# Performance work log

Measured on AMD Instinct MI355X. Metric: run time of the kernel, lower is better.

Reference implementation:

```python
import jax, jax.numpy as jnp
import numpy as np

B, S, D = 2, 2048, 1024
H_Q, H_KV, DK, DV = 16, 8, 64, 64
R = H_Q // H_KV  # q heads per kv head (GQA)
THETA = 10000.0


def setup_inputs() -> dict:
    key = jax.random.key(0)
    ks = jax.random.split(key, 12)
    inv_freq = 1.0 / (THETA ** (jnp.arange(0, DK, 2, dtype=jnp.float32) / DK))  # [DK/2]
    angles = jnp.arange(S, dtype=jnp.float32)[:, None] * inv_freq[None, :]      # [S, DK/2]
    scale = 0.02
    return {
        "x": jax.random.normal(ks[0], (B, S, D), jnp.float32),
        "Wq": jax.random.normal(ks[1], (D, H_Q * DK), jnp.float32) * scale,
        "bq": jnp.zeros((H_Q * DK,), jnp.float32),
        "Wk": jax.random.normal(ks[2], (D, H_KV * DK), jnp.float32) * scale,
        "bk": jnp.zeros((H_KV * DK,), jnp.float32),
        "Wv": jax.random.normal(ks[3], (D, H_KV * DV), jnp.float32) * scale,
        "bv": jnp.zeros((H_KV * DV,), jnp.float32),
        "Wo": jax.random.normal(ks[4], (H_Q * DV, D), jnp.float32) * scale,
        "bo": jnp.zeros((D,), jnp.float32),
        "freqs_cos": jnp.cos(angles),
        "freqs_sin": jnp.sin(angles),
        "attention_mask": jax.random.bernoulli(ks[5], 0.9, (B, S)),  # True = real token
    }


def _rope(t, cos, sin):
    # t: [B, S, H, Dh]; cos/sin: [S, Dh/2]. Complex rotation on interleaved pairs.
    tp = t.reshape(*t.shape[:-1], -1, 2)
    x1, x2 = tp[..., 0], tp[..., 1]
    c = cos[None, :, None, :]
    s = sin[None, :, None, :]
    o1 = x1 * c - x2 * s
    o2 = x1 * s + x2 * c
    return jnp.stack([o1, o2], axis=-1).reshape(t.shape)


def reference(x, Wq, bq, Wk, bk, Wv, bv, Wo, bo, freqs_cos, freqs_sin, attention_mask):
    b, s, _ = x.shape
    q = (x @ Wq + bq).reshape(b, s, H_Q, DK)
    k = (x @ Wk + bk).reshape(b, s, H_KV, DK)
    v = (x @ Wv + bv).reshape(b, s, H_KV, DV)
    q = _rope(q, freqs_cos, freqs_sin)
    k = _rope(k, freqs_cos, freqs_sin)
    q = q.transpose(0, 2, 1, 3)                      # [B, Hq, S, DK]
    k = jnp.repeat(k.transpose(0, 2, 1, 3), R, axis=1)  # GQA expand -> [B, Hq, S, DK]
    v = jnp.repeat(v.transpose(0, 2, 1, 3), R, axis=1)  # [B, Hq, S, DV]
    causal = jnp.tril(jnp.ones((s, s), dtype=bool))
    # Module does logical_or(padding, causal) -- replicated faithfully.
    mask = jnp.logical_or(attention_mask[:, None, None, :], causal[None, None])
    scale = 1.0 / jnp.sqrt(jnp.float32(DK))
    scores = jnp.einsum('bhqd,bhkd->bhqk', q, k) * scale
    scores = jnp.where(mask, scores, -jnp.inf)
    attn = jax.nn.softmax(scores, axis=-1)
    out = jnp.einsum('bhqk,bhkd->bhqd', attn, v)
    out = out.transpose(0, 2, 1, 3).reshape(b, s, H_Q * DV)
    return out @ Wo + bo
```

## Files before the change

### kernel.cpp

```cpp
#include <hip/hip_runtime.h>
#include <hip/hip_bf16.h>
#include <math.h>

typedef __attribute__((ext_vector_type(8))) short bf16x8;
typedef __attribute__((ext_vector_type(4))) float f32x4;

#define OFF_XB  0ull
#define OFF_WT  (8ull<<20)
#define OFF_WO  (12ull<<20)
#define OFF_QB  (14ull<<20)
#define OFF_KB  (22ull<<20)
#define OFF_VT  (26ull<<20)
#define OFF_AO  (30ull<<20)
#define OFF_MB  (38ull<<20)

#define QSCALE 0.18033688056680276f

__device__ inline unsigned pack_bf162(float a, float b) {
    __hip_bfloat162 t = __float22bfloat162_rn(make_float2(a, b));
    return *(unsigned*)&t;
}

__device__ inline float exp2_fast(float x) {
    float r;
    asm("v_exp_f32 %0, %1" : "=v"(r) : "v"(x));
    return r;
}

__device__ inline void gload16(const void* g, void* l) {
    __builtin_amdgcn_global_load_lds(
        (const __attribute__((address_space(1))) void*)g,
        (__attribute__((address_space(3))) void*)l, 16, 0, 0);
}

__launch_bounds__(256)
__global__ void prep_kernel(const float* __restrict__ x,
                            const float* __restrict__ Wq, const float* __restrict__ Wk,
                            const float* __restrict__ Wv, const float* __restrict__ Wo,
                            const void* __restrict__ mraw,
                            __hip_bfloat16* __restrict__ XB,
                            __hip_bfloat16* __restrict__ WT,
                            __hip_bfloat16* __restrict__ WoT,
                            float* __restrict__ mbias) {
    __shared__ float T[32][33];
    __shared__ int bad01, badf;
    const int tid = threadIdx.x;
    const int bid = blockIdx.x;
    if (bid < 1024) {
        const int base = bid * 4096;
#pragma unroll
        for (int i = 0; i < 4; ++i) {
            const int e = base + (i * 256 + tid) * 4;
            const float4 v = *(const float4*)&x[e];
            uint2 pk;
            pk.x = pack_bf162(v.x, v.y);
            pk.y = pack_bf162(v.z, v.w);
            *(uint2*)&XB[e] = pk;
        }
    } else if (bid < 4096) {
        const float* src; int ldn, nbase; __hip_bfloat16* dst; int n0, k0;
        if (bid < 3072) {
            const int tb = bid - 1024;
            const int kt = tb >> 6, nt = tb & 63;
            n0 = nt * 32; k0 = kt * 32; dst = WT;
            if (n0 < 1024)      { src = Wq; ldn = 1024; nbase = n0; }
            else if (n0 < 1536) { src = Wk; ldn = 512;  nbase = n0 - 1024; }
            else                { src = Wv; ldn = 512;  nbase = n0 - 1536; }
        } else {
            const int tb = bid - 3072;
            const int kt = tb >> 5, nt = tb & 31;
            n0 = nt * 32; k0 = kt * 32; dst = WoT;
            src = Wo; ldn = 1024; nbase = n0;
        }
        const int c = tid & 31, r0 = tid >> 5;
#pragma unroll
        for (int i = 0; i < 4; ++i)
            T[r0 + 8 * i][c] = src[(size_t)(k0 + r0 + 8 * i) * ldn + nbase + c];
        __syncthreads();
#pragma unroll
        for (int i = 0; i < 4; ++i) {
            const int nn = r0 + 8 * i;
            dst[(size_t)(n0 + nn) * 1024 + k0 + c] = __float2bfloat16(T[c][nn]);
        }
    } else {
        if (tid == 0) { bad01 = 0; badf = 0; }
        __syncthreads();
        const unsigned* w = (const unsigned*)mraw;
#pragma unroll
        for (int i = 0; i < 4; ++i) {
            const unsigned v = w[tid * 4 + i];
            if (v > 1u) atomicAdd(&bad01, 1);
            if (v != 0u && v != 0x3F800000u) atomicAdd(&badf, 1);
        }
        __syncthreads();
        const int fmt = (bad01 == 0) ? 0 : ((badf == 0) ? 1 : 2);
        for (int i = tid; i < 4096; i += 256) {
            bool on;
            if (fmt == 2) on = (((const unsigned char*)mraw)[i] != 0);
            else          on = (w[i] != 0u);
            mbias[i] = on ? 0.f : -1e30f;
        }
    }
}

__launch_bounds__(256)
__global__ void qkv_mfma_kernel(const __hip_bfloat16* __restrict__ XB,
                                const __hip_bfloat16* __restrict__ WT,
                                const float* __restrict__ bq, const float* __restrict__ bk,
                                const float* __restrict__ bv,
                                const float* __restrict__ fc, const float* __restrict__ fs,
                                __hip_bfloat16* __restrict__ QB,
                                __hip_bfloat16* __restrict__ KB,
                                __hip_bfloat16* __restrict__ VT) {
    __shared__ __attribute__((aligned(16))) char Asm[16384];
    __shared__ __attribute__((aligned(16))) char Bsm[16384];
    const int tid = threadIdx.x;
    const int lane = tid & 63, wid = tid >> 6;
    const int c = lane & 15, g = lane >> 4;
    const int n0 = blockIdx.x * 128, m0 = blockIdx.y * 128;
    const int wn = (wid >> 1) * 64, wm = (wid & 1) * 64;

    f32x4 acc[4][4];
#pragma unroll
    for (int ni = 0; ni < 4; ++ni)
#pragma unroll
        for (int mj = 0; mj < 4; ++mj) acc[ni][mj] = f32x4{0.f, 0.f, 0.f, 0.f};

    for (int kt = 0; kt < 16; ++kt) {
        const int k0 = kt * 64;
#pragma unroll
        for (int rnd = 0; rnd < 4; ++rnd) {
            const int off = rnd * 4096 + wid * 1024 + lane * 16;
            const int row = off >> 7;
            const int chunk = ((off >> 4) & 7) ^ (row & 7);
            gload16((const char*)WT + ((size_t)(n0 + row) * 1024 + k0 + chunk * 8) * 2,
                    Asm + rnd * 4096 + wid * 1024);
            gload16((const char*)XB + ((size_t)(m0 + row) * 1024 + k0 + chunk * 8) * 2,
                    Bsm + rnd * 4096 + wid * 1024);
        }
        __syncthreads();
#pragma unroll
        for (int ks = 0; ks < 2; ++ks) {
            bf16x8 af[4], bfr[4];
#pragma unroll
            for (int t = 0; t < 4; ++t) {
                const int sl = ((g + 4 * ks) ^ (c & 7)) << 4;
                af[t]  = *(const bf16x8*)(Asm + (wn + 16 * t + c) * 128 + sl);
                bfr[t] = *(const bf16x8*)(Bsm + (wm + 16 * t + c) * 128 + sl);
            }
#pragma unroll
            for (int ni = 0; ni < 4; ++ni)
#pragma unroll
                for (int mj = 0; mj < 4; ++mj)
                    acc[ni][mj] = __builtin_amdgcn_mfma_f32_16x16x32_bf16(
                        af[ni], bfr[mj], acc[ni][mj], 0, 0, 0);
        }
        __syncthreads();
    }

#pragma unroll
    for (int ni = 0; ni < 4; ++ni) {
        const int nb = n0 + wn + 16 * ni + 4 * g;
        const float* bias; int nloc;
        if (nb < 1024)      { bias = bq; nloc = nb; }
        else if (nb < 1536) { bias = bk; nloc = nb - 1024; }
        else                { bias = bv; nloc = nb - 1536; }
        const float4 b4 = *(const float4*)&bias[nloc];
        const int h = nloc >> 6, dk = nb & 63;
#pragma unroll
        for (int mj = 0; mj < 4; ++mj) {
            const int tok = m0 + wm + 16 * mj + c;
            const int bb = tok >> 11, sp = tok & 2047;
            float v0 = acc[ni][mj][0] + b4.x;
            float v1 = acc[ni][mj][1] + b4.y;
            float v2 = acc[ni][mj][2] + b4.z;
            float v3 = acc[ni][mj][3] + b4.w;
            if (nb < 1536) {
                const int p = sp * 32 + (dk >> 1);
                const float c0 = fc[p], s0 = fs[p];
                const float c1 = fc[p + 1], s1 = fs[p + 1];
                float o0 = v0 * c0 - v1 * s0, o1 = v0 * s0 + v1 * c0;
                float o2 = v2 * c1 - v3 * s1, o3 = v2 * s1 + v3 * c1;
                uint2 pk;
                if (nb < 1024) {
                    o0 *= QSCALE; o1 *= QSCALE; o2 *= QSCALE; o3 *= QSCALE;
                    pk.x = pack_bf162(o0, o1); pk.y = pack_bf162(o2, o3);
                    *(uint2*)&QB[(size_t)((bb * 16 + h) * 2048 + sp) * 64 + dk] = pk;
                } else {
                    pk.x = pack_bf162(o0, o1); pk.y = pack_bf162(o2, o3);
                    *(uint2*)&KB[(size_t)((bb * 8 + h) * 2048 + sp) * 64 + dk] = pk;
                }
            } else {
                const size_t vb = (size_t)((bb * 8 + h) * 64 + dk) * 2048 + sp;
                VT[vb]          = __float2bfloat16(v0);
                VT[vb + 2048]   = __float2bfloat16(v1);
                VT[vb + 4096]   = __float2bfloat16(v2);
                VT[vb + 6144]   = __float2bfloat16(v3);
            }
        }
    }
}

__launch_bounds__(256)
__global__ void out_mfma_kernel(const __hip_bfloat16* __restrict__ AOB,
                                const __hip_bfloat16* __restrict__ WoT,
                                const float* __restrict__ bo,
                                float* __restrict__ out) {
    __shared__ __attribute__((aligned(16))) char Asm[16384];
    __shared__ __attribute__((aligned(16))) char Bsm[16384];
    const int tid = threadIdx.x;
    const int lane = tid & 63, wid = tid >> 6;
    const int c = lane & 15, g = lane >> 4;
    const int n0 = blockIdx.x * 128, m0 = blockIdx.y * 128;
    const int wn = (wid >> 1) * 64, wm = (wid & 1) * 64;

    f32x4 acc[4][4];
#pragma unroll
    for (int ni = 0; ni < 4; ++ni)
#pragma unroll
        for (int mj = 0; mj < 4; ++mj) acc[ni][mj] = f32x4{0.f, 0.f, 0.f, 0.f};

    for (int kt = 0; kt < 16; ++kt) {
        const int k0 = kt * 64;
#pragma unroll
        for (int rnd = 0; rnd < 4; ++rnd) {
            const int off = rnd * 4096 + wid * 1024 + lane * 16;
            const int row = off >> 7;
            const int chunk = ((off >> 4) & 7) ^ (row & 7);
            gload16((const char*)WoT + ((size_t)(n0 + row) * 1024 + k0 + chunk * 8) * 2,
                    Asm + rnd * 4096 + wid * 1024);
            gload16((const char*)AOB + ((size_t)(m0 + row) * 1024 + k0 + chunk * 8) * 2,
                    Bsm + rnd * 4096 + wid * 1024);
        }
        __syncthreads();
#pragma unroll
        for (int ks = 0; ks < 2; ++ks) {
            bf16x8 af[4], bfr[4];
#pragma unroll
            for (int t = 0; t < 4; ++t) {
                const int sl = ((g + 4 * ks) ^ (c & 7)) << 4;
                af[t]  = *(const bf16x8*)(Asm + (wn + 16 * t + c) * 128 + sl);
                bfr[t] = *(const bf16x8*)(Bsm + (wm + 16 * t + c) * 128 + sl);
            }
#pragma unroll
            for (int ni = 0; ni < 4; ++ni)
#pragma unroll
                for (int mj = 0; mj < 4; ++mj)
                    acc[ni][mj] = __builtin_amdgcn_mfma_f32_16x16x32_bf16(
                        af[ni], bfr[mj], acc[ni][mj], 0, 0, 0);
        }
        __syncthreads();
    }
#pragma unroll
    for (int ni = 0; ni < 4; ++ni) {
        const int nb = n0 + wn + 16 * ni + 4 * g;
        const float4 b4 = *(const float4*)&bo[nb];
#pragma unroll
        for (int mj = 0; mj < 4; ++mj) {
            const int tok = m0 + wm + 16 * mj + c;
            const f32x4 a = acc[ni][mj];
            const float4 st = make_float4(a[0] + b4.x, a[1] + b4.y,
                                          a[2] + b4.z, a[3] + b4.w);
            *(float4*)&out[(size_t)tok * 1024 + nb] = st;
        }
    }
}


#define STAGE(BUFSEL, K0_) do {                                                  \
    _Pragma("unroll") for (int rnd_ = 0; rnd_ < 2; ++rnd_) {                     \
        const int off_ = rnd_ * 4096 + tid * 16;                                 \
        const int row_ = off_ >> 7;                                              \
        const int ch_  = ((off_ >> 4) & 7) ^ (row_ & 7);                         \
        gload16(Kh + (size_t)((K0_) + row_) * 64 + ch_ * 8,                      \
                Ksm + (BUFSEL) * 8192 + rnd_ * 4096 + wid * 1024);               \
        gload16(Vh + (size_t)row_ * 2048 + (K0_) + ch_ * 8,                      \
                Vsm + (BUFSEL) * 8192 + rnd_ * 4096 + wid * 1024);               \
    }                                                                            \
} while (0)

__launch_bounds__(256)
__global__ void attn_kernel(const __hip_bfloat16* __restrict__ QB,
                            const __hip_bfloat16* __restrict__ KB,
                            const __hip_bfloat16* __restrict__ VT,
                            const float* __restrict__ maskb,
                            __hip_bfloat16* __restrict__ AOB) {
    __shared__ __attribute__((aligned(16))) char Ksm[16384];
    __shared__ __attribute__((aligned(16))) char Vsm[16384];
    __shared__ float bias_sm[2048];
    __shared__ char  P_lds[4][4096];

    const int tid  = threadIdx.x;
    const int lane = tid & 63, wid = tid >> 6;
    const int c = lane & 15, g = lane >> 4;

    const int bid = blockIdx.x;
    const int o_  = (bid & 7) * 64 + (bid >> 3);
    const int qx = o_ & 15, h = (o_ >> 4) & 15, b = o_ >> 8;
    const int qb = qx * 128 + wid * 32;

    const __hip_bfloat16* Qh = QB + (size_t)(b * 16 + h)       * 2048 * 64;
    const __hip_bfloat16* Kh = KB + (size_t)(b * 8 + (h >> 1)) * 2048 * 64;
    const __hip_bfloat16* Vh = VT + (size_t)(b * 8 + (h >> 1)) * 64 * 2048;

    {
        const float* mb = maskb + b * 2048;
        for (int i = tid; i < 512; i += 256)
            *(float4*)&bias_sm[4 * i] = *(const float4*)&mb[4 * i];
    }
    STAGE(0, 0);

    bf16x8 bq[2][2];
#pragma unroll
    for (int rt = 0; rt < 2; ++rt)
#pragma unroll
        for (int ks = 0; ks < 2; ++ks)
            bq[rt][ks] = *(const bf16x8*)&Qh[(size_t)(qb + 16 * rt + c) * 64
                                             + 32 * ks + 8 * g];
    __syncthreads();

    f32x4 o[2][4];
#pragma unroll
    for (int rt = 0; rt < 2; ++rt)
#pragma unroll
        for (int mt = 0; mt < 4; ++mt) o[rt][mt] = f32x4{0.f, 0.f, 0.f, 0.f};
    float m_[2] = {-INFINITY, -INFINITY}, l_[2] = {0.f, 0.f};

    char* Pw = &P_lds[wid][0];
    const int swz = (c & 7) << 4;

    int cur = 0;
    for (int kt = 0; kt < 32; ++kt) {
        const int k0 = kt * 64;
        if (kt < 31) {
            STAGE(cur ^ 1, k0 + 64);
            asm volatile("s_waitcnt vmcnt(4)" ::: "memory");
        } else {
            asm volatile("s_waitcnt vmcnt(0)" ::: "memory");
        }
        __builtin_amdgcn_sched_barrier(0);
        __builtin_amdgcn_s_barrier();
        __builtin_amdgcn_sched_barrier(0);

        const char* Kc = Ksm + cur * 8192;
        const char* Vc = Vsm + cur * 8192;

        bf16x8 ak[4][2];
#pragma unroll
        for (int mt = 0; mt < 4; ++mt)
#pragma unroll
            for (int ks = 0; ks < 2; ++ks)
                ak[mt][ks] = *(const bf16x8*)(Kc + (16 * mt + c) * 128
                                              + (((g + 4 * ks) ^ (c & 7)) << 4));
        f32x4 st[2][4];
#pragma unroll
        for (int rt = 0; rt < 2; ++rt)
#pragma unroll
            for (int mt = 0; mt < 4; ++mt) {
                f32x4 z = f32x4{0.f, 0.f, 0.f, 0.f};
                z = __builtin_amdgcn_mfma_f32_16x16x32_bf16(ak[mt][0], bq[rt][0], z, 0, 0, 0);
                z = __builtin_amdgcn_mfma_f32_16x16x32_bf16(ak[mt][1], bq[rt][1], z, 0, 0, 0);
                st[rt][mt] = z;
            }

        bf16x8 av[4][2];
#pragma unroll
        for (int mt = 0; mt < 4; ++mt)
#pragma unroll
            for (int ks = 0; ks < 2; ++ks)
                av[mt][ks] = *(const bf16x8*)(Vc + (16 * mt + c) * 128
                                              + (((g + 4 * ks) ^ (c & 7)) << 4));

#pragma unroll
        for (int rt = 0; rt < 2; ++rt) {
            float pmax = -INFINITY;
            if (k0 + 63 <= qb) {
#pragma unroll
                for (int mt = 0; mt < 4; ++mt)
#pragma unroll
                    for (int r = 0; r < 4; ++r)
                        pmax = fmaxf(pmax, st[rt][mt][r]);
            } else if (k0 > qb + 31) {
#pragma unroll
                for (int mt = 0; mt < 4; ++mt) {
                    const float4 bv4 = *(const float4*)&bias_sm[k0 + 16 * mt + 4 * g];
                    st[rt][mt][0] += bv4.x; st[rt][mt][1] += bv4.y;
                    st[rt][mt][2] += bv4.z; st[rt][mt][3] += bv4.w;
#pragma unroll
                    for (int r = 0; r < 4; ++r)
                        pmax = fmaxf(pmax, st[rt][mt][r]);
                }
            } else {
                const int qg = qb + 16 * rt + c;
#pragma unroll
                for (int mt = 0; mt < 4; ++mt) {
                    const float4 bv4 = *(const float4*)&bias_sm[k0 + 16 * mt + 4 * g];
                    const float bvr[4] = {bv4.x, bv4.y, bv4.z, bv4.w};
#pragma unroll
                    for (int r = 0; r < 4; ++r) {
                        const int kg = k0 + 16 * mt + 4 * g + r;
                        st[rt][mt][r] += (kg <= qg) ? 0.f : bvr[r];
                        pmax = fmaxf(pmax, st[rt][mt][r]);
                    }
                }
            }
            pmax = fmaxf(pmax, __shfl_xor(pmax, 16));
            pmax = fmaxf(pmax, __shfl_xor(pmax, 32));
            if (!__all(pmax <= m_[rt] + 11.5f)) {
                const float mn = fmaxf(m_[rt], pmax);
                const float alpha = exp2_fast(m_[rt] - mn);
                m_[rt] = mn; l_[rt] *= alpha;
#pragma unroll
                for (int mt = 0; mt < 4; ++mt) o[rt][mt] *= alpha;
            }
            float ts = 0.f;
#pragma unroll
            for (int mt = 0; mt < 4; ++mt)
#pragma unroll
                for (int r = 0; r < 4; ++r) {
                    const float e = exp2_fast(st[rt][mt][r] - m_[rt]);
                    st[rt][mt][r] = e; ts += e;
                }
            ts += __shfl_xor(ts, 16);
            ts += __shfl_xor(ts, 32);
            l_[rt] += ts;

            char* Pr = Pw + rt * 2048 + c * 128;
#pragma unroll
            for (int mt = 0; mt < 4; ++mt) {
                const unsigned w0 = pack_bf162(st[rt][mt][0], st[rt][mt][1]);
                const unsigned w1 = pack_bf162(st[rt][mt][2], st[rt][mt][3]);
                *(unsigned long long*)(Pr + ((32 * mt + 8 * g) ^ swz)) =
                    (unsigned long long)w0 | ((unsigned long long)w1 << 32);
            }
        }

#pragma unroll
        for (int rt = 0; rt < 2; ++rt) {
            const char* Pr = Pw + rt * 2048 + c * 128;
            const bf16x8 pb0 = *(const bf16x8*)(Pr + ((16 * g) ^ swz));
            const bf16x8 pb1 = *(const bf16x8*)(Pr + ((64 + 16 * g) ^ swz));
#pragma unroll
            for (int mt = 0; mt < 4; ++mt) {
                o[rt][mt] = __builtin_amdgcn_mfma_f32_16x16x32_bf16(av[mt][0], pb0, o[rt][mt], 0, 0, 0);
                o[rt][mt] = __builtin_amdgcn_mfma_f32_16x16x32_bf16(av[mt][1], pb1, o[rt][mt], 0, 0, 0);
            }
        }

        __builtin_amdgcn_sched_barrier(0);
        __builtin_amdgcn_s_barrier();
        __builtin_amdgcn_sched_barrier(0);
        cur ^= 1;
    }

#pragma unroll
    for (int rt = 0; rt < 2; ++rt) {
        const float inv = 1.f / l_[rt];
        const size_t tok = (size_t)(b * 2048 + qb + 16 * rt + c);
#pragma unroll
        for (int mt = 0; mt < 4; ++mt) {
            uint2 pk;
            pk.x = pack_bf162(o[rt][mt][0] * inv, o[rt][mt][1] * inv);
            pk.y = pack_bf162(o[rt][mt][2] * inv, o[rt][mt][3] * inv);
            *(uint2*)&AOB[tok * 1024 + h * 64 + 16 * mt + 4 * g] = pk;
        }
    }
}

extern "C" void kernel_launch(void* const* d_in, const int* in_sizes, int n_in,
                              void* d_out, int out_size, void* d_ws, size_t ws_size,
                              hipStream_t stream) {
    const float* x  = (const float*)d_in[0];
    const float* Wq = (const float*)d_in[1];
    const float* bq = (const float*)d_in[2];
    const float* Wk = (const float*)d_in[3];
    const float* bk = (const float*)d_in[4];
    const float* Wv = (const float*)d_in[5];
    const float* bv = (const float*)d_in[6];
    const float* Wo = (const float*)d_in[7];
    const float* bo = (const float*)d_in[8];
    const float* fc = (const float*)d_in[9];
    const float* fs = (const float*)d_in[10];
    const void*  am = d_in[11];

    char* ws = (char*)d_ws;
    __hip_bfloat16* XB  = (__hip_bfloat16*)(ws + OFF_XB);
    __hip_bfloat16* WT  = (__hip_bfloat16*)(ws + OFF_WT);
    __hip_bfloat16* WoT = (__hip_bfloat16*)(ws + OFF_WO);
    __hip_bfloat16* QB  = (__hip_bfloat16*)(ws + OFF_QB);
    __hip_bfloat16* KB  = (__hip_bfloat16*)(ws + OFF_KB);
    __hip_bfloat16* VT  = (__hip_bfloat16*)(ws + OFF_VT);
    __hip_bfloat16* AOB = (__hip_bfloat16*)(ws + OFF_AO);
    float* mbias = (float*)(ws + OFF_MB);
    float* out   = (float*)d_out;

    hipLaunchKernelGGL(prep_kernel, dim3(4097), dim3(256), 0, stream,
                       x, Wq, Wk, Wv, Wo, am, XB, WT, WoT, mbias);
    hipLaunchKernelGGL(qkv_mfma_kernel, dim3(16, 32), dim3(256), 0, stream,
                       XB, WT, bq, bk, bv, fc, fs, QB, KB, VT);
    hipLaunchKernelGGL(attn_kernel, dim3(512), dim3(256), 0, stream,
                       QB, KB, VT, mbias, AOB);
    hipLaunchKernelGGL(out_mfma_kernel, dim3(8, 32), dim3(256), 0, stream,
                       AOB, WoT, bo, out);
}
```

Before: 147.0 us.

## Load mask bias from global per tile, shrink P LDS, add MFMA priority hints

Removes the per-block shared-memory copy of the padding bias. Bias is now read from global memory only on tiles that need it, and the mask checks are tightened per 16-row subtile. The P staging buffer is halved by reusing one per-wave slot for both row tiles, with each P-V MFMA issued right after its P write. s_setprio raises wave priority around the MFMA blocks. Less LDS may allow more resident blocks, at the cost of extra global loads on the critical path and a possible write-then-read hazard on the reused P buffer.

```diff
diff --git a/kernel.cpp b/kernel.cpp
--- a/kernel.cpp
+++ b/kernel.cpp
@@ -287,8 +287,7 @@
                             __hip_bfloat16* __restrict__ AOB) {
     __shared__ __attribute__((aligned(16))) char Ksm[16384];
     __shared__ __attribute__((aligned(16))) char Vsm[16384];
-    __shared__ float bias_sm[2048];
-    __shared__ char  P_lds[4][4096];
+    __shared__ char P_lds[4][2048];
 
     const int tid  = threadIdx.x;
     const int lane = tid & 63, wid = tid >> 6;
@@ -302,12 +301,8 @@
     const __hip_bfloat16* Qh = QB + (size_t)(b * 16 + h)       * 2048 * 64;
     const __hip_bfloat16* Kh = KB + (size_t)(b * 8 + (h >> 1)) * 2048 * 64;
     const __hip_bfloat16* Vh = VT + (size_t)(b * 8 + (h >> 1)) * 64 * 2048;
-
-    {
-        const float* mb = maskb + b * 2048;
-        for (int i = tid; i < 512; i += 256)
-            *(float4*)&bias_sm[4 * i] = *(const float4*)&mb[4 * i];
-    }
+    const float* mb = maskb + b * 2048;
+
     STAGE(0, 0);
 
     bf16x8 bq[2][2];
@@ -326,7 +321,7 @@
         for (int mt = 0; mt < 4; ++mt) o[rt][mt] = f32x4{0.f, 0.f, 0.f, 0.f};
     float m_[2] = {-INFINITY, -INFINITY}, l_[2] = {0.f, 0.f};
 
-    char* Pw = &P_lds[wid][0];
+    char* Pr = &P_lds[wid][0] + c * 128;
     const int swz = (c & 7) << 4;
 
     int cur = 0;
@@ -352,6 +347,16 @@
             for (int ks = 0; ks < 2; ++ks)
                 ak[mt][ks] = *(const bf16x8*)(Kc + (16 * mt + c) * 128
                                               + (((g + 4 * ks) ^ (c & 7)) << 4));
+
+        const bool needb = (k0 + 63 > qb);
+        float4 biasv[4];
+        if (needb) {
+#pragma unroll
+            for (int mt = 0; mt < 4; ++mt)
+                biasv[mt] = *(const float4*)&mb[k0 + 16 * mt + 4 * g];
+        }
+
+        __builtin_amdgcn_s_setprio(1);
         f32x4 st[2][4];
 #pragma unroll
         for (int rt = 0; rt < 2; ++rt)
@@ -362,6 +367,7 @@
                 z = __builtin_amdgcn_mfma_f32_16x16x32_bf16(ak[mt][1], bq[rt][1], z, 0, 0, 0);
                 st[rt][mt] = z;
             }
+        __builtin_amdgcn_s_setprio(0);
 
         bf16x8 av[4][2];
 #pragma unroll
@@ -373,29 +379,29 @@
 
 #pragma unroll
         for (int rt = 0; rt < 2; ++rt) {
+            const int qw = qb + 16 * rt;
             float pmax = -INFINITY;
-            if (k0 + 63 <= qb) {
+            if (k0 + 63 <= qw) {
 #pragma unroll
                 for (int mt = 0; mt < 4; ++mt)
 #pragma unroll
                     for (int r = 0; r < 4; ++r)
                         pmax = fmaxf(pmax, st[rt][mt][r]);
-            } else if (k0 > qb + 31) {
+            } else if (k0 > qw + 15) {
 #pragma unroll
                 for (int mt = 0; mt < 4; ++mt) {
-                    const float4 bv4 = *(const float4*)&bias_sm[k0 + 16 * mt + 4 * g];
-                    st[rt][mt][0] += bv4.x; st[rt][mt][1] += bv4.y;
-                    st[rt][mt][2] += bv4.z; st[rt][mt][3] += bv4.w;
+                    st[rt][mt][0] += biasv[mt].x; st[rt][mt][1] += biasv[mt].y;
+                    st[rt][mt][2] += biasv[mt].z; st[rt][mt][3] += biasv[mt].w;
 #pragma unroll
                     for (int r = 0; r < 4; ++r)
                         pmax = fmaxf(pmax, st[rt][mt][r]);
                 }
             } else {
-                const int qg = qb + 16 * rt + c;
+                const int qg = qw + c;
 #pragma unroll
                 for (int mt = 0; mt < 4; ++mt) {
-                    const float4 bv4 = *(const float4*)&bias_sm[k0 + 16 * mt + 4 * g];
-                    const float bvr[4] = {bv4.x, bv4.y, bv4.z, bv4.w};
+                    const float bvr[4] = {biasv[mt].x, biasv[mt].y,
+                                          biasv[mt].z, biasv[mt].w};
 #pragma unroll
                     for (int r = 0; r < 4; ++r) {
                         const int kg = k0 + 16 * mt + 4 * g + r;
@@ -425,7 +431,6 @@
             ts += __shfl_xor(ts, 32);
             l_[rt] += ts;
 
-            char* Pr = Pw + rt * 2048 + c * 128;
 #pragma unroll
             for (int mt = 0; mt < 4; ++mt) {
                 const unsigned w0 = pack_bf162(st[rt][mt][0], st[rt][mt][1]);
@@ -433,18 +438,15 @@
                 *(unsigned long long*)(Pr + ((32 * mt + 8 * g) ^ swz)) =
                     (unsigned long long)w0 | ((unsigned long long)w1 << 32);
             }
-        }
-
-#pragma unroll
-        for (int rt = 0; rt < 2; ++rt) {
-            const char* Pr = Pw + rt * 2048 + c * 128;
             const bf16x8 pb0 = *(const bf16x8*)(Pr + ((16 * g) ^ swz));
             const bf16x8 pb1 = *(const bf16x8*)(Pr + ((64 + 16 * g) ^ swz));
+            __builtin_amdgcn_s_setprio(1);
 #pragma unroll
             for (int mt = 0; mt < 4; ++mt) {
                 o[rt][mt] = __builtin_amdgcn_mfma_f32_16x16x32_bf16(av[mt][0], pb0, o[rt][mt], 0, 0, 0);
                 o[rt][mt] = __builtin_amdgcn_mfma_f32_16x16x32_bf16(av[mt][1], pb1, o[rt][mt], 0, 0, 0);
             }
+            __builtin_amdgcn_s_setprio(0);
         }
 
         __builtin_amdgcn_sched_barrier(0);
```

Measured after the change: 145.4 us. No clear change (-1.1%).
